# Kernel optimization log

Hardware: AMD Instinct MI355X
Metric: run time of the kernel (lower is better)

The kernel has to match this reference:

```python
import jax, jax.numpy as jnp
import numpy as np

NEG_SLOPE = 0.2
TAU_MRF = 1.0
N_NODES = 100000
PROJ_DIM = 128
GAT_DIM = 64
N_EDGES = 1000000


def setup_inputs() -> dict:
    key = jax.random.key(0)
    ks = jax.random.split(key, 8)
    z_beh = jax.random.normal(ks[0], (N_NODES, PROJ_DIM), dtype=jnp.float32)
    z_pref = jax.random.normal(ks[1], (N_NODES, PROJ_DIM), dtype=jnp.float32)
    edge_index = jax.random.randint(ks[2], (2, N_EDGES), 0, N_NODES, dtype=jnp.int64)
    # xavier_uniform for [GAT_DIM, PROJ_DIM] linear weights
    lim_w = float(np.sqrt(6.0 / (PROJ_DIM + GAT_DIM)))
    W_b = jax.random.uniform(ks[3], (GAT_DIM, PROJ_DIM), minval=-lim_w, maxval=lim_w, dtype=jnp.float32)
    W_p = jax.random.uniform(ks[4], (GAT_DIM, PROJ_DIM), minval=-lim_w, maxval=lim_w, dtype=jnp.float32)
    # xavier_uniform on view(1, 2D): fan_in=1? torch treats [1, 2D] -> fan_in=2D, fan_out=1
    lim_a = float(np.sqrt(6.0 / (1 + 2 * GAT_DIM)))
    a_b = jax.random.uniform(ks[5], (2 * GAT_DIM,), minval=-lim_a, maxval=lim_a, dtype=jnp.float32)
    a_p = jax.random.uniform(ks[6], (2 * GAT_DIM,), minval=-lim_a, maxval=lim_a, dtype=jnp.float32)
    gamma_b = jnp.zeros((), dtype=jnp.float32)
    gamma_p = jnp.zeros((), dtype=jnp.float32)
    return {"z_beh": z_beh, "z_pref": z_pref, "W_b": W_b, "W_p": W_p,
            "a_b": a_b, "a_p": a_p, "gamma_b": gamma_b, "gamma_p": gamma_p,
            "edge_index_undirected": edge_index}


def _sym_score(h, a, src, dst, neg_slope):
    # e_ij = leaky_relu((cat[h_src, h_dst]) . a). Split a to avoid materializing
    # the [E, 2D] concat: dot each node once, then gather scalars per edge.
    D = h.shape[-1]
    si = h @ a[:D]   # [N] contribution of left slot
    sj = h @ a[D:]   # [N] contribution of right slot
    e_ij = jax.nn.leaky_relu(si[src] + sj[dst], negative_slope=neg_slope)
    e_ji = jax.nn.leaky_relu(si[dst] + sj[src], negative_slope=neg_slope)
    return 0.5 * (e_ij + e_ji)


def reference(z_beh, z_pref, W_b, W_p, a_b, a_p, gamma_b, gamma_p, edge_index_undirected):
    src = edge_index_undirected[0]
    dst = edge_index_undirected[1]
    h_b = z_beh @ W_b.T   # [N, D]
    h_p = z_pref @ W_p.T  # [N, D]
    s_b = _sym_score(h_b, a_b, src, dst, NEG_SLOPE)  # [E]
    s_p = _sym_score(h_p, a_p, src, dst, NEG_SLOPE)  # [E]
    w = jax.nn.softmax(jnp.stack([gamma_b, gamma_p]))
    s = w[0] * s_b + w[1] * s_p
    alpha_ij = jax.nn.sigmoid(s / TAU_MRF)
    return alpha_ij
```

## Files before the change

### kernel.cpp

```cpp
#include <hip/hip_runtime.h>
#include <hip/hip_bf16.h>

#define NEG_SLOPE 0.2f

typedef float f32x4 __attribute__((ext_vector_type(4)));
typedef int   i32x4 __attribute__((ext_vector_type(4)));

__global__ void compute_v_kernel(const float* __restrict__ W_b,
                                 const float* __restrict__ W_p,
                                 const float* __restrict__ a_b,
                                 const float* __restrict__ a_p,
                                 float* __restrict__ v) {
    const int t  = threadIdx.x;
    const int p  = t & 127;
    const int ch = t >> 7;
    const float* W = ch ? W_p : W_b;
    const float* a = ch ? a_p : a_b;
    float acc1 = 0.f, acc2 = 0.f;
    #pragma unroll
    for (int d = 0; d < 64; ++d) {
        const float w = W[d * 128 + p];
        acc1 += w * a[d];
        acc2 += w * a[64 + d];
    }
    v[(2 * ch + 0) * 128 + p] = acc1;
    v[(2 * ch + 1) * 128 + p] = acc2;
}

__global__ void __launch_bounds__(256) node_scores_kernel(
        const f32x4* __restrict__ zb4,
        const f32x4* __restrict__ zp4,
        const float* __restrict__ v,
        float*       __restrict__ tab,
        int n_nodes) {
    const int t    = threadIdx.x;
    const int lane = t & 63;
    const int h    = lane >> 5;
    const int c    = lane & 31;
    const int wave   = (blockIdx.x * blockDim.x + t) >> 6;
    const int nwaves = (gridDim.x * blockDim.x) >> 6;
    const int npairs = (n_nodes + 1) >> 1;

    const f32x4 v1b = *reinterpret_cast<const f32x4*>(v + 0 * 128 + 4 * c);
    const f32x4 v2b = *reinterpret_cast<const f32x4*>(v + 1 * 128 + 4 * c);
    const f32x4 v1p = *reinterpret_cast<const f32x4*>(v + 2 * 128 + 4 * c);
    const f32x4 v2p = *reinterpret_cast<const f32x4*>(v + 3 * 128 + 4 * c);

    const bool hiB = (c & 16) != 0;
    const bool hiJ = (c & 8)  != 0;

    for (int pr = wave; pr < npairs; pr += nwaves) {
        int node = 2 * pr + h;
        const int valid = node < n_nodes;
        if (!valid) node = n_nodes - 1;
        const size_t base = (size_t)node * 32 + c;
        const f32x4 zb = zb4[base];
        const f32x4 zp = zp4[base];
        float sib = zb.x * v1b.x + zb.y * v1b.y + zb.z * v1b.z + zb.w * v1b.w;
        float sjb = zb.x * v2b.x + zb.y * v2b.y + zb.z * v2b.z + zb.w * v2b.w;
        float sip = zp.x * v1p.x + zp.y * v1p.y + zp.z * v1p.z + zp.w * v1p.w;
        float sjp = zp.x * v2p.x + zp.y * v2p.y + zp.z * v2p.z + zp.w * v2p.w;

        float g1 = hiB ? sib : sip;
        float r1 = __shfl_xor(g1, 16);
        float acc_i = (hiB ? sip : sib) + r1;
        float g2 = hiB ? sjb : sjp;
        float r2 = __shfl_xor(g2, 16);
        float acc_j = (hiB ? sjp : sjb) + r2;

        float g3 = hiJ ? acc_i : acc_j;
        float r3 = __shfl_xor(g3, 8);
        float acc = (hiJ ? acc_j : acc_i) + r3;

        acc += __shfl_xor(acc, 4);
        acc += __shfl_xor(acc, 2);
        acc += __shfl_xor(acc, 1);

        if ((c & 7) == 0 && valid) {
            tab[(size_t)node * 4 + (c >> 3)] = acc;
        }
    }
}

__device__ __forceinline__ float lrelu(float x) {
    return x >= 0.f ? x : NEG_SLOPE * x;
}

__device__ __forceinline__ float edge_score(const f32x4 ts, const f32x4 td,
                                            float w0, float w1) {
    const float sb = 0.5f * (lrelu(ts.x + td.y) + lrelu(td.x + ts.y));
    const float sp = 0.5f * (lrelu(ts.z + td.w) + lrelu(td.z + ts.w));
    const float sc = w0 * sb + w1 * sp;
    return 1.f / (1.f + __expf(-sc));
}

__global__ void __launch_bounds__(256) edge_scores_kernel(
        const int*   __restrict__ src,
        const int*   __restrict__ dst,
        const f32x4* __restrict__ tab,
        const float* __restrict__ gamma_b,
        const float* __restrict__ gamma_p,
        float*       __restrict__ out,
        int n_edges) {
    const float gb = *gamma_b;
    const float gp = *gamma_p;
    const float w0 = 1.f / (1.f + __expf(gp - gb));
    const float w1 = 1.f - w0;

    const int n_quads = n_edges >> 2;
    const int stride  = gridDim.x * blockDim.x;
    const int gid     = blockIdx.x * blockDim.x + threadIdx.x;

    const i32x4* src4 = (const i32x4*)src;
    const i32x4* dst4 = (const i32x4*)dst;
    f32x4*       out4 = (f32x4*)out;

    for (int i = gid; i < n_quads; i += stride) {
        const i32x4 s = src4[i];
        const i32x4 d = dst4[i];
        f32x4 r;
        r.x = edge_score(tab[s.x], tab[d.x], w0, w1);
        r.y = edge_score(tab[s.y], tab[d.y], w0, w1);
        r.z = edge_score(tab[s.z], tab[d.z], w0, w1);
        r.w = edge_score(tab[s.w], tab[d.w], w0, w1);
        out4[i] = r;
    }
    const int tail_base = n_quads << 2;
    for (int e = tail_base + gid; e < n_edges; e += stride) {
        out[e] = edge_score(tab[src[e]], tab[dst[e]], w0, w1);
    }
}

extern "C" void kernel_launch(void* const* d_in, const int* in_sizes, int n_in,
                              void* d_out, int out_size, void* d_ws, size_t ws_size,
                              hipStream_t stream) {
    const float* z_beh  = (const float*)d_in[0];
    const float* z_pref = (const float*)d_in[1];
    const float* W_b    = (const float*)d_in[2];
    const float* W_p    = (const float*)d_in[3];
    const float* a_b    = (const float*)d_in[4];
    const float* a_p    = (const float*)d_in[5];
    const float* g_b    = (const float*)d_in[6];
    const float* g_p    = (const float*)d_in[7];
    const int*   ei     = (const int*)d_in[8];

    const int n_nodes = in_sizes[0] / 128;
    const int n_edges = in_sizes[8] / 2;

    float* v   = (float*)d_ws;
    float* tab = (float*)((char*)d_ws + 2048);

    compute_v_kernel<<<1, 256, 0, stream>>>(W_b, W_p, a_b, a_p, v);

    node_scores_kernel<<<2048, 256, 0, stream>>>(
        (const f32x4*)z_beh, (const f32x4*)z_pref, v, tab, n_nodes);

    const int n_quads = n_edges >> 2;
    int eblocks = (n_quads + 255) / 256;
    if (eblocks > 2048) eblocks = 2048;
    if (eblocks < 1) eblocks = 1;
    edge_scores_kernel<<<eblocks, 256, 0, stream>>>(
        ei, ei + n_edges, (const f32x4*)tab, g_b, g_p, (float*)d_out, n_edges);
}
```

Baseline: 38.61 us.

## Fuse projection-vector computation into node kernel and rebalance edge gather width

Folds the tiny W·a projection kernel into the node-score kernel: each 1024-thread block recomputes the four 128-wide projection vectors into shared memory, which removes one kernel launch and its dependency. The node loop now handles two node pairs per iteration so more loads are in flight, and the launch moves to 512 blocks of 1024 threads. The edge kernel processes two edges per thread instead of four, with up to 4096 blocks, to expose more parallel gathers. The cost is redundant per-block weight reads and a shared-memory reduction, plus narrower vector loads for the edge indices.

```diff
diff --git a/kernel.cpp b/kernel.cpp
--- a/kernel.cpp
+++ b/kernel.cpp
@@ -4,81 +4,99 @@
 #define NEG_SLOPE 0.2f
 
 typedef float f32x4 __attribute__((ext_vector_type(4)));
-typedef int   i32x4 __attribute__((ext_vector_type(4)));
 
-__global__ void compute_v_kernel(const float* __restrict__ W_b,
-                                 const float* __restrict__ W_p,
-                                 const float* __restrict__ a_b,
-                                 const float* __restrict__ a_p,
-                                 float* __restrict__ v) {
-    const int t  = threadIdx.x;
-    const int p  = t & 127;
-    const int ch = t >> 7;
-    const float* W = ch ? W_p : W_b;
-    const float* a = ch ? a_p : a_b;
-    float acc1 = 0.f, acc2 = 0.f;
-    #pragma unroll
-    for (int d = 0; d < 64; ++d) {
-        const float w = W[d * 128 + p];
-        acc1 += w * a[d];
-        acc2 += w * a[64 + d];
-    }
-    v[(2 * ch + 0) * 128 + p] = acc1;
-    v[(2 * ch + 1) * 128 + p] = acc2;
+__device__ __forceinline__ float fold_reduce(float sib, float sjb,
+                                             float sip, float sjp,
+                                             bool hiB, bool hiJ) {
+    float g1 = hiB ? sib : sip;
+    float r1 = __shfl_xor(g1, 16);
+    float acc_i = (hiB ? sip : sib) + r1;
+    float g2 = hiB ? sjb : sjp;
+    float r2 = __shfl_xor(g2, 16);
+    float acc_j = (hiB ? sjp : sjb) + r2;
+    float g3 = hiJ ? acc_i : acc_j;
+    float r3 = __shfl_xor(g3, 8);
+    float acc = (hiJ ? acc_j : acc_i) + r3;
+    acc += __shfl_xor(acc, 4);
+    acc += __shfl_xor(acc, 2);
+    acc += __shfl_xor(acc, 1);
+    return acc;
 }
 
-__global__ void __launch_bounds__(256) node_scores_kernel(
+__device__ __forceinline__ float dot4(const f32x4 z, const f32x4 v) {
+    return z.x * v.x + z.y * v.y + z.z * v.z + z.w * v.w;
+}
+
+__global__ void __launch_bounds__(1024) fused_node_kernel(
+        const float* __restrict__ W_b,
+        const float* __restrict__ W_p,
+        const float* __restrict__ a_b,
+        const float* __restrict__ a_p,
         const f32x4* __restrict__ zb4,
         const f32x4* __restrict__ zp4,
-        const float* __restrict__ v,
         float*       __restrict__ tab,
         int n_nodes) {
-    const int t    = threadIdx.x;
-    const int lane = t & 63;
+    __shared__ float vsh[4][128];
+    __shared__ float psh[1024];
+
+    const int tid = threadIdx.x;
+    {
+        const int q   = tid >> 9;
+        const int r   = tid & 511;
+        const int vec = r >> 7;
+        const int p   = r & 127;
+        const float* W = (vec >= 2) ? W_p : W_b;
+        const float* a = ((vec >= 2) ? a_p : a_b) + (vec & 1) * 64 + 32 * q;
+        const float* Wc = W + (32 * q) * 128 + p;
+        float acc = 0.f;
+        #pragma unroll
+        for (int k = 0; k < 32; ++k)
+            acc += Wc[k * 128] * a[k];
+        psh[tid] = acc;
+    }
+    __syncthreads();
+    if (tid < 512)
+        vsh[tid >> 7][tid & 127] = psh[tid] + psh[512 + tid];
+    __syncthreads();
+
+    const int lane = tid & 63;
     const int h    = lane >> 5;
     const int c    = lane & 31;
-    const int wave   = (blockIdx.x * blockDim.x + t) >> 6;
+    const int wave   = (blockIdx.x * blockDim.x + tid) >> 6;
     const int nwaves = (gridDim.x * blockDim.x) >> 6;
     const int npairs = (n_nodes + 1) >> 1;
 
-    const f32x4 v1b = *reinterpret_cast<const f32x4*>(v + 0 * 128 + 4 * c);
-    const f32x4 v2b = *reinterpret_cast<const f32x4*>(v + 1 * 128 + 4 * c);
-    const f32x4 v1p = *reinterpret_cast<const f32x4*>(v + 2 * 128 + 4 * c);
-    const f32x4 v2p = *reinterpret_cast<const f32x4*>(v + 3 * 128 + 4 * c);
+    const f32x4 v1b = *reinterpret_cast<const f32x4*>(&vsh[0][4 * c]);
+    const f32x4 v2b = *reinterpret_cast<const f32x4*>(&vsh[1][4 * c]);
+    const f32x4 v1p = *reinterpret_cast<const f32x4*>(&vsh[2][4 * c]);
+    const f32x4 v2p = *reinterpret_cast<const f32x4*>(&vsh[3][4 * c]);
 
     const bool hiB = (c & 16) != 0;
     const bool hiJ = (c & 8)  != 0;
+    const bool wr  = (c & 7) == 0;
+    const int  comp = c >> 3;
 
-    for (int pr = wave; pr < npairs; pr += nwaves) {
-        int node = 2 * pr + h;
-        const int valid = node < n_nodes;
-        if (!valid) node = n_nodes - 1;
-        const size_t base = (size_t)node * 32 + c;
-        const f32x4 zb = zb4[base];
-        const f32x4 zp = zp4[base];
-        float sib = zb.x * v1b.x + zb.y * v1b.y + zb.z * v1b.z + zb.w * v1b.w;
-        float sjb = zb.x * v2b.x + zb.y * v2b.y + zb.z * v2b.z + zb.w * v2b.w;
-        float sip = zp.x * v1p.x + zp.y * v1p.y + zp.z * v1p.z + zp.w * v1p.w;
-        float sjp = zp.x * v2p.x + zp.y * v2p.y + zp.z * v2p.z + zp.w * v2p.w;
+    for (int pr = wave; pr < npairs; pr += 2 * nwaves) {
+        const int pr2 = pr + nwaves;
+        int node1 = 2 * pr + h;
+        const bool valid1 = node1 < n_nodes;
+        if (!valid1) node1 = n_nodes - 1;
+        const f32x4 zb1 = zb4[node1 * 32 + c];
+        const f32x4 zp1 = zp4[node1 * 32 + c];
+        int node2 = 2 * pr2 + h;
+        const bool run2   = pr2 < npairs;
+        bool valid2 = run2 && (node2 < n_nodes);
+        if (!valid2) node2 = n_nodes - 1;
+        const f32x4 zb2 = zb4[node2 * 32 + c];
+        const f32x4 zp2 = zp4[node2 * 32 + c];
 
-        float g1 = hiB ? sib : sip;
-        float r1 = __shfl_xor(g1, 16);
-        float acc_i = (hiB ? sip : sib) + r1;
-        float g2 = hiB ? sjb : sjp;
-        float r2 = __shfl_xor(g2, 16);
-        float acc_j = (hiB ? sjp : sjb) + r2;
+        float acc1 = fold_reduce(dot4(zb1, v1b), dot4(zb1, v2b),
+                                 dot4(zp1, v1p), dot4(zp1, v2p), hiB, hiJ);
+        if (wr && valid1) tab[node1 * 4 + comp] = acc1;
 
-        float g3 = hiJ ? acc_i : acc_j;
-        float r3 = __shfl_xor(g3, 8);
-        float acc = (hiJ ? acc_j : acc_i) + r3;
-
-        acc += __shfl_xor(acc, 4);
-        acc += __shfl_xor(acc, 2);
-        acc += __shfl_xor(acc, 1);
-
-        if ((c & 7) == 0 && valid) {
-            tab[(size_t)node * 4 + (c >> 3)] = acc;
-        }
+        float acc2 = fold_reduce(dot4(zb2, v1b), dot4(zb2, v2b),
+                                 dot4(zp2, v1p), dot4(zp2, v2p), hiB, hiJ);
+        if (wr && valid2) tab[node2 * 4 + comp] = acc2;
     }
 }
 
@@ -107,25 +125,27 @@
     const float w0 = 1.f / (1.f + __expf(gp - gb));
     const float w1 = 1.f - w0;
 
-    const int n_quads = n_edges >> 2;
-    const int stride  = gridDim.x * blockDim.x;
-    const int gid     = blockIdx.x * blockDim.x + threadIdx.x;
+    const int n_half = n_edges >> 1;
+    const int stride = gridDim.x * blockDim.x;
+    const int gid    = blockIdx.x * blockDim.x + threadIdx.x;
 
-    const i32x4* src4 = (const i32x4*)src;
-    const i32x4* dst4 = (const i32x4*)dst;
-    f32x4*       out4 = (f32x4*)out;
+    const int2* src2 = (const int2*)src;
+    const int2* dst2 = (const int2*)dst;
+    float2*     out2 = (float2*)out;
 
-    for (int i = gid; i < n_quads; i += stride) {
-        const i32x4 s = src4[i];
-        const i32x4 d = dst4[i];
-        f32x4 r;
-        r.x = edge_score(tab[s.x], tab[d.x], w0, w1);
-        r.y = edge_score(tab[s.y], tab[d.y], w0, w1);
-        r.z = edge_score(tab[s.z], tab[d.z], w0, w1);
-        r.w = edge_score(tab[s.w], tab[d.w], w0, w1);
-        out4[i] = r;
+    for (int i = gid; i < n_half; i += stride) {
+        const int2 s = src2[i];
+        const int2 d = dst2[i];
+        const f32x4 ts0 = tab[s.x];
+        const f32x4 td0 = tab[d.x];
+        const f32x4 ts1 = tab[s.y];
+        const f32x4 td1 = tab[d.y];
+        float2 r;
+        r.x = edge_score(ts0, td0, w0, w1);
+        r.y = edge_score(ts1, td1, w0, w1);
+        out2[i] = r;
     }
-    const int tail_base = n_quads << 2;
+    const int tail_base = n_half << 1;
     for (int e = tail_base + gid; e < n_edges; e += stride) {
         out[e] = edge_score(tab[src[e]], tab[dst[e]], w0, w1);
     }
@@ -147,17 +167,15 @@
     const int n_nodes = in_sizes[0] / 128;
     const int n_edges = in_sizes[8] / 2;
 
-    float* v   = (float*)d_ws;
-    float* tab = (float*)((char*)d_ws + 2048);
+    float* tab = (float*)d_ws;
 
-    compute_v_kernel<<<1, 256, 0, stream>>>(W_b, W_p, a_b, a_p, v);
+    fused_node_kernel<<<512, 1024, 0, stream>>>(
+        W_b, W_p, a_b, a_p,
+        (const f32x4*)z_beh, (const f32x4*)z_pref, tab, n_nodes);
 
-    node_scores_kernel<<<2048, 256, 0, stream>>>(
-        (const f32x4*)z_beh, (const f32x4*)z_pref, v, tab, n_nodes);
-
-    const int n_quads = n_edges >> 2;
-    int eblocks = (n_quads + 255) / 256;
-    if (eblocks > 2048) eblocks = 2048;
+    const int n_half = n_edges >> 1;
+    int eblocks = (n_half + 255) / 256;
+    if (eblocks > 4096) eblocks = 4096;
     if (eblocks < 1) eblocks = 1;
     edge_scores_kernel<<<eblocks, 256, 0, stream>>>(
         ei, ei + n_edges, (const f32x4*)tab, g_b, g_p, (float*)d_out, n_edges);
```

Measured after the change: 36.15 us. -6.4%, faster.
